# Performance work log

Measured on AMD Instinct MI355X. Metric: run time of the kernel, lower is better.

Reference implementation:

```python
import jax, jax.numpy as jnp
import numpy as np

N = 50000
E = 800000
D_IN = 128
D_H = 128
D_OUT = 128
EPS = 1e-5


def setup_inputs() -> dict:
    key = jax.random.key(0)
    ks = jax.random.split(key, 16)
    s = 1.0 / np.sqrt(D_IN)
    inp = {
        "x": jax.random.normal(ks[0], (N, D_IN), dtype=jnp.float32),
        "src": jax.random.randint(ks[1], (E,), 0, N, dtype=jnp.int32),
        "dst": jax.random.randint(ks[2], (E,), 0, N, dtype=jnp.int32),
        # SAGEConv layer 1 (in->hidden): fc_self, fc_neigh, bias
        "Ws1": jax.random.uniform(ks[3], (D_IN, D_H), jnp.float32, -s, s),
        "Wn1": jax.random.uniform(ks[4], (D_IN, D_H), jnp.float32, -s, s),
        "b1": jnp.zeros((D_H,), jnp.float32),
        # BN1
        "gamma1": jnp.ones((D_H,), jnp.float32),
        "beta1": jnp.zeros((D_H,), jnp.float32),
        # SAGEConv layer 2 (hidden->hidden)
        "Ws2": jax.random.uniform(ks[5], (D_H, D_H), jnp.float32, -s, s),
        "Wn2": jax.random.uniform(ks[6], (D_H, D_H), jnp.float32, -s, s),
        "b2": jnp.zeros((D_H,), jnp.float32),
        # BN2
        "gamma2": jnp.ones((D_H,), jnp.float32),
        "beta2": jnp.zeros((D_H,), jnp.float32),
        # SAGEConv layer 3 (hidden->out)
        "Ws3": jax.random.uniform(ks[7], (D_H, D_OUT), jnp.float32, -s, s),
        "Wn3": jax.random.uniform(ks[8], (D_H, D_OUT), jnp.float32, -s, s),
        "b3": jnp.zeros((D_OUT,), jnp.float32),
    }
    return inp


def _sage_conv(x, src, dst, Ws, Wn, b):
    # mean aggregation of neighbor (src) features onto dst nodes
    agg = jax.ops.segment_sum(x[src], dst, num_segments=N)  # [N, d]
    deg = jax.ops.segment_sum(jnp.ones((E,), x.dtype), dst, num_segments=N)
    h_neigh = agg / jnp.maximum(deg, 1.0)[:, None]  # isolated nodes -> 0
    return x @ Ws + h_neigh @ Wn + b


def _batch_norm(h, gamma, beta):
    mu = jnp.mean(h, axis=0)
    var = jnp.mean(jnp.square(h - mu), axis=0)  # biased var (torch BN)
    return (h - mu) * jax.lax.rsqrt(var + EPS) * gamma + beta


def reference(x, src, dst, Ws1, Wn1, b1, gamma1, beta1,
              Ws2, Wn2, b2, gamma2, beta2, Ws3, Wn3, b3):
    h = jax.nn.relu(_batch_norm(_sage_conv(x, src, dst, Ws1, Wn1, b1), gamma1, beta1))
    # dropout is identity at inference
    h = jax.nn.relu(_batch_norm(_sage_conv(h, src, dst, Ws2, Wn2, b2), gamma2, beta2))
    return _sage_conv(h, src, dst, Ws3, Wn3, b3)
```

## Files before the change

### kernel.cpp

```cpp
#include <hip/hip_runtime.h>

#define N_NODES 50000
#define NEDGE   800000
#define D       128
#define EPS     1e-5f
#define NT      3125
#define NUNITS  800000
#define NHALF   ((size_t)N_NODES * 64)

typedef __attribute__((ext_vector_type(8))) short bf16x8;
typedef __attribute__((ext_vector_type(4))) float f32x4;
typedef __attribute__((ext_vector_type(8))) unsigned short u16x8;

__device__ inline uint32_t bfhi(float f) {
    uint32_t u = __float_as_uint(f);
    u += 0x7fffu + ((u >> 16) & 1u);
    return u >> 16;
}
__device__ inline float bff(uint32_t h) { return __uint_as_float(h << 16); }

__global__ __launch_bounds__(256) void k_deg(const int* __restrict__ dst,
                                             int* __restrict__ degi) {
    int e = blockIdx.x * 256 + threadIdx.x;
    if (e < NEDGE) atomicAdd(&degi[dst[e]], 1);
}

__global__ __launch_bounds__(256) void k_scan1(const int* __restrict__ degi,
                                               int* __restrict__ offs,
                                               int* __restrict__ bsum) {
    __shared__ int s[256];
    int tid = threadIdx.x;
    int i = blockIdx.x * 256 + tid;
    int v = (i < N_NODES) ? degi[i] : 0;
    s[tid] = v;
    __syncthreads();
    for (int d = 1; d < 256; d <<= 1) {
        int t = (tid >= d) ? s[tid - d] : 0;
        __syncthreads();
        s[tid] += t;
        __syncthreads();
    }
    if (i < N_NODES) offs[i] = s[tid] - v;
    if (tid == 255) bsum[blockIdx.x] = s[255];
}

__global__ __launch_bounds__(256) void k_scan2(int* __restrict__ bsum, int nb) {
    __shared__ int s[256];
    int tid = threadIdx.x;
    int v = (tid < nb) ? bsum[tid] : 0;
    s[tid] = v;
    __syncthreads();
    for (int d = 1; d < 256; d <<= 1) {
        int t = (tid >= d) ? s[tid - d] : 0;
        __syncthreads();
        s[tid] += t;
        __syncthreads();
    }
    if (tid < nb) bsum[tid] = s[tid] - v;
}

__global__ __launch_bounds__(256) void k_scan3(const int* __restrict__ degi,
                                               const int* __restrict__ bsum,
                                               int* __restrict__ offs,
                                               int* __restrict__ cursor,
                                               float* __restrict__ invdeg) {
    int i = blockIdx.x * 256 + threadIdx.x;
    if (i < N_NODES) {
        int o = offs[i] + bsum[blockIdx.x];
        offs[i] = o;
        cursor[i] = o;
        int dg = degi[i];
        invdeg[i] = 1.0f / (float)(dg > 0 ? dg : 1);
    }
    if (i == 0 && blockIdx.x == 0) offs[N_NODES] = NEDGE;
}

__global__ __launch_bounds__(256) void k_fill(const int* __restrict__ src,
                                              const int* __restrict__ dst,
                                              int* __restrict__ cursor,
                                              int* __restrict__ csr) {
    int e = blockIdx.x * 256 + threadIdx.x;
    if (e < NEDGE) {
        int p = atomicAdd(&cursor[dst[e]], 1);
        csr[p] = src[e];
    }
}

__global__ __launch_bounds__(256) void k_tobf16(const float* __restrict__ X,
                                                unsigned short* __restrict__ PH,
                                                unsigned short* __restrict__ PL,
                                                unsigned short* __restrict__ XG) {
    int flat = blockIdx.x * 256 + threadIdx.x;
    if (flat >= NUNITS) return;
    int tb = flat >> 8;
    int kc = (flat >> 6) & 3;
    int l = flat & 63;
    int row = tb * 16 + (l & 15);
    int col = kc * 32 + (l >> 4) * 8;
    const float* p = X + (size_t)row * D + col;
    float4 a = *reinterpret_cast<const float4*>(p);
    float4 b = *reinterpret_cast<const float4*>(p + 4);
    float f[8] = {a.x, a.y, a.z, a.w, b.x, b.y, b.z, b.w};
    u16x8 oh, ol;
#pragma unroll
    for (int i = 0; i < 8; ++i) {
        uint32_t h = bfhi(f[i]);
        oh[i] = (unsigned short)h;
        ol[i] = (unsigned short)bfhi(f[i] - bff(h));
    }
    *reinterpret_cast<u16x8*>(PH + (size_t)flat * 8) = oh;
    *reinterpret_cast<u16x8*>(PL + (size_t)flat * 8) = ol;
    *reinterpret_cast<u16x8*>(XG + (size_t)(col >> 6) * NHALF + (size_t)row * 64 + (col & 63)) = oh;
}

__global__ __launch_bounds__(256) void k_act(const float* __restrict__ H,
                                             const float* __restrict__ scale,
                                             const float* __restrict__ shift,
                                             unsigned short* __restrict__ PH,
                                             unsigned short* __restrict__ PL,
                                             unsigned short* __restrict__ XG) {
    int flat = blockIdx.x * 256 + threadIdx.x;
    if (flat >= NUNITS) return;
    int tb = flat >> 8;
    int kc = (flat >> 6) & 3;
    int l = flat & 63;
    int row = tb * 16 + (l & 15);
    int col = kc * 32 + (l >> 4) * 8;
    const float* p = H + (size_t)row * D + col;
    float4 a = *reinterpret_cast<const float4*>(p);
    float4 b = *reinterpret_cast<const float4*>(p + 4);
    float4 s0 = *reinterpret_cast<const float4*>(scale + col);
    float4 s1 = *reinterpret_cast<const float4*>(scale + col + 4);
    float4 h0 = *reinterpret_cast<const float4*>(shift + col);
    float4 h1 = *reinterpret_cast<const float4*>(shift + col + 4);
    float f[8];
    f[0] = fmaxf(a.x * s0.x + h0.x, 0.f); f[1] = fmaxf(a.y * s0.y + h0.y, 0.f);
    f[2] = fmaxf(a.z * s0.z + h0.z, 0.f); f[3] = fmaxf(a.w * s0.w + h0.w, 0.f);
    f[4] = fmaxf(b.x * s1.x + h1.x, 0.f); f[5] = fmaxf(b.y * s1.y + h1.y, 0.f);
    f[6] = fmaxf(b.z * s1.z + h1.z, 0.f); f[7] = fmaxf(b.w * s1.w + h1.w, 0.f);
    u16x8 oh, ol;
#pragma unroll
    for (int i = 0; i < 8; ++i) {
        uint32_t h = bfhi(f[i]);
        oh[i] = (unsigned short)h;
        ol[i] = (unsigned short)bfhi(f[i] - bff(h));
    }
    *reinterpret_cast<u16x8*>(PH + (size_t)flat * 8) = oh;
    *reinterpret_cast<u16x8*>(PL + (size_t)flat * 8) = ol;
    *reinterpret_cast<u16x8*>(XG + (size_t)(col >> 6) * NHALF + (size_t)row * 64 + (col & 63)) = oh;
}

__global__ __launch_bounds__(256) void k_agg(const unsigned short* __restrict__ XG,
                                             const int* __restrict__ offs,
                                             const int* __restrict__ csr,
                                             const float* __restrict__ invdeg,
                                             unsigned short* __restrict__ HNH,
                                             unsigned short* __restrict__ HNL) {
    int bid = blockIdx.x;
    int half = (bid >> 2) & 1;
    int nb = (bid >> 3) * 4 + (bid & 3);
    if (nb >= 1563) return;
    int n = nb * 32 + (threadIdx.x >> 3);
    if (n >= N_NODES) return;
    int c = (threadIdx.x & 7) * 8;
    const unsigned short* XP = XG + (size_t)half * NHALF;

    int e0 = offs[n], e1 = offs[n + 1];
    float a0[8], a1[8];
#pragma unroll
    for (int i = 0; i < 8; ++i) { a0[i] = 0.f; a1[i] = 0.f; }

    int e = e0;
    for (; e + 2 <= e1; e += 2) {
        int s0i = csr[e], s1i = csr[e + 1];
        u16x8 v0 = *reinterpret_cast<const u16x8*>(XP + (size_t)s0i * 64 + c);
        u16x8 v1 = *reinterpret_cast<const u16x8*>(XP + (size_t)s1i * 64 + c);
#pragma unroll
        for (int i = 0; i < 8; ++i) {
            a0[i] += bff((unsigned short)v0[i]);
            a1[i] += bff((unsigned short)v1[i]);
        }
    }
    if (e < e1) {
        int s0i = csr[e];
        u16x8 v0 = *reinterpret_cast<const u16x8*>(XP + (size_t)s0i * 64 + c);
#pragma unroll
        for (int i = 0; i < 8; ++i)
            a0[i] += bff((unsigned short)v0[i]);
    }
    float id = invdeg[n];
    u16x8 oh, ol;
#pragma unroll
    for (int i = 0; i < 8; ++i) {
        float m = (a0[i] + a1[i]) * id;
        uint32_t h = bfhi(m);
        oh[i] = (unsigned short)h;
        ol[i] = (unsigned short)bfhi(m - bff(h));
    }
    int gc = half * 64 + c;
    int kc = gc >> 5;
    int l = (n & 15) + ((gc >> 3) & 3) * 16;
    size_t unit = ((size_t)(n >> 4) * 4 + kc) * 64 + l;
    *reinterpret_cast<u16x8*>(HNH + unit * 8) = oh;
    *reinterpret_cast<u16x8*>(HNL + unit * 8) = ol;
}

__global__ __launch_bounds__(256) void k_wprep(const float* __restrict__ W0,
                                               const float* __restrict__ W1,
                                               const float* __restrict__ W2,
                                               const float* __restrict__ W3,
                                               const float* __restrict__ W4,
                                               const float* __restrict__ W5,
                                               unsigned short* __restrict__ wt) {
    int mat = blockIdx.x >> 6;
    const float* srcs[6] = {W0, W1, W2, W3, W4, W5};
    const float* W = srcs[mat];
    int t = (blockIdx.x & 63) * 256 + threadIdx.x;
    int k = t >> 7;
    int n = t & 127;
    float w = W[k * 128 + n];
    uint32_t h = bfhi(w);
    uint32_t l = bfhi(w - bff(h));
    unsigned short* base = wt + (size_t)mat * 32768;
    base[n * 128 + k] = (unsigned short)h;
    base[16384 + n * 128 + k] = (unsigned short)l;
}

__global__ __launch_bounds__(256, 4) void k_mm(const unsigned short* __restrict__ PH,
                                               const unsigned short* __restrict__ PL,
                                               const unsigned short* __restrict__ HNH,
                                               const unsigned short* __restrict__ HNL,
                                               const unsigned short* __restrict__ WsT,
                                               const unsigned short* __restrict__ WnT,
                                               const float* __restrict__ bias,
                                               float* __restrict__ OUT,
                                               int doStats,
                                               float* __restrict__ sums) {
    const int tid = threadIdx.x;
    const int lane = tid & 63;
    const int wave = tid >> 6;
    const int mlo = lane & 15;
    const int g = lane >> 4;
    const int ch = blockIdx.x & 1;
    const int t0 = (blockIdx.x >> 1) * 4;
    const int row0 = t0 * 16;
    const int col = ch * 64 + wave * 16 + mlo;
    const float bcol = bias[col];

    f32x4 acc[4];
#pragma unroll
    for (int s = 0; s < 4; ++s) acc[s] = (f32x4){0.f, 0.f, 0.f, 0.f};

#pragma unroll
    for (int kc = 0; kc < 4; ++kc) {
        int ko = kc * 32 + g * 8;
        bf16x8 wsh = *reinterpret_cast<const bf16x8*>(WsT + (size_t)col * 128 + ko);
        bf16x8 wsl = *reinterpret_cast<const bf16x8*>(WsT + 16384 + (size_t)col * 128 + ko);
        bf16x8 wnh = *reinterpret_cast<const bf16x8*>(WnT + (size_t)col * 128 + ko);
        bf16x8 wnl = *reinterpret_cast<const bf16x8*>(WnT + 16384 + (size_t)col * 128 + ko);
#pragma unroll
        for (int s = 0; s < 4; ++s) {
            int t = t0 + s;
            u16x8 xh, xl, ah, al;
            if (t < NT) {
                size_t idx = (((size_t)t * 4 + kc) * 64 + lane) * 8;
                xh = *reinterpret_cast<const u16x8*>(PH + idx);
                xl = *reinterpret_cast<const u16x8*>(PL + idx);
                ah = *reinterpret_cast<const u16x8*>(HNH + idx);
                al = *reinterpret_cast<const u16x8*>(HNL + idx);
            } else {
                u16x8 z = {0, 0, 0, 0, 0, 0, 0, 0};
                xh = z; xl = z; ah = z; al = z;
            }
            bf16x8 bxh = *(bf16x8*)&xh, bxl = *(bf16x8*)&xl;
            bf16x8 bah = *(bf16x8*)&ah, bal = *(bf16x8*)&al;
            acc[s] = __builtin_amdgcn_mfma_f32_16x16x32_bf16(bxh, wsh, acc[s], 0, 0, 0);
            acc[s] = __builtin_amdgcn_mfma_f32_16x16x32_bf16(bxh, wsl, acc[s], 0, 0, 0);
            acc[s] = __builtin_amdgcn_mfma_f32_16x16x32_bf16(bxl, wsh, acc[s], 0, 0, 0);
            acc[s] = __builtin_amdgcn_mfma_f32_16x16x32_bf16(bah, wnh, acc[s], 0, 0, 0);
            acc[s] = __builtin_amdgcn_mfma_f32_16x16x32_bf16(bah, wnl, acc[s], 0, 0, 0);
            acc[s] = __builtin_amdgcn_mfma_f32_16x16x32_bf16(bal, wnh, acc[s], 0, 0, 0);
        }
    }

    float cs = 0.f, cq = 0.f;
#pragma unroll
    for (int s = 0; s < 4; ++s) {
#pragma unroll
        for (int r = 0; r < 4; ++r) {
            int grow = row0 + s * 16 + g * 4 + r;
            if (grow < N_NODES) {
                float v = acc[s][r] + bcol;
                OUT[(size_t)grow * D + col] = v;
                cs += v; cq += v * v;
            }
        }
    }
    if (doStats) {
        cs += __shfl_xor(cs, 16); cs += __shfl_xor(cs, 32);
        cq += __shfl_xor(cq, 16); cq += __shfl_xor(cq, 32);
        if (lane < 16) {
            atomicAdd(&sums[col], cs);
            atomicAdd(&sums[128 + col], cq);
        }
    }
}

__global__ void k_bnfin(const float* __restrict__ sums,
                        const float* __restrict__ gamma,
                        const float* __restrict__ beta,
                        float* __restrict__ scale,
                        float* __restrict__ shift) {
    int c = threadIdx.x;
    const float invN = 1.0f / (float)N_NODES;
    float mu = sums[c] * invN;
    float var = sums[128 + c] * invN - mu * mu;
    float s = gamma[c] * rsqrtf(var + EPS);
    scale[c] = s;
    shift[c] = beta[c] - mu * s;
}

extern "C" void kernel_launch(void* const* d_in, const int* in_sizes, int n_in,
                              void* d_out, int out_size, void* d_ws, size_t ws_size,
                              hipStream_t stream) {
    const float* x   = (const float*)d_in[0];
    const int*   src = (const int*)d_in[1];
    const int*   dst = (const int*)d_in[2];
    const float* Ws1 = (const float*)d_in[3];
    const float* Wn1 = (const float*)d_in[4];
    const float* b1  = (const float*)d_in[5];
    const float* g1  = (const float*)d_in[6];
    const float* be1 = (const float*)d_in[7];
    const float* Ws2 = (const float*)d_in[8];
    const float* Wn2 = (const float*)d_in[9];
    const float* b2  = (const float*)d_in[10];
    const float* g2  = (const float*)d_in[11];
    const float* be2 = (const float*)d_in[12];
    const float* Ws3 = (const float*)d_in[13];
    const float* Wn3 = (const float*)d_in[14];
    const float* b3  = (const float*)d_in[15];
    float* out = (float*)d_out;

    char* p = (char*)d_ws;
    auto alloc = [&](size_t bytes) -> char* {
        char* r = p;
        p += (bytes + 255) & ~(size_t)255;
        return r;
    };
    unsigned short* pfh = (unsigned short*)alloc((size_t)NUNITS * 16);
    unsigned short* pfl = (unsigned short*)alloc((size_t)NUNITS * 16);
    unsigned short* xg  = (unsigned short*)alloc((size_t)N_NODES * D * 2);
    unsigned short* hnh = (unsigned short*)alloc((size_t)NUNITS * 16);
    unsigned short* hnl = (unsigned short*)alloc((size_t)NUNITS * 16);
    float* hbuf   = (float*)alloc((size_t)N_NODES * D * 4);
    int*   csr    = (int*)alloc((size_t)NEDGE * 4);
    int*   offs   = (int*)alloc((size_t)(N_NODES + 1) * 4);
    int*   cursor = (int*)alloc((size_t)N_NODES * 4);
    int*   degi   = (int*)alloc((size_t)N_NODES * 4);
    float* invdeg = (float*)alloc((size_t)N_NODES * 4);
    int*   bsum   = (int*)alloc(1024);
    float* sums   = (float*)alloc(256 * 4);
    float* scale  = (float*)alloc(128 * 4);
    float* shift  = (float*)alloc(128 * 4);
    unsigned short* wt = (unsigned short*)alloc((size_t)6 * 32768 * 2);

    const int NB_E = (NEDGE + 255) / 256;
    const int NB_N = (N_NODES + 255) / 256;
    const int NB_A = 3128;
    const int NB_M = 2 * ((N_NODES + 63) / 64);
    const int NB_T = (NUNITS + 255) / 256;

    const unsigned short* WsT1 = wt + 0 * 32768;
    const unsigned short* WnT1 = wt + 1 * 32768;
    const unsigned short* WsT2 = wt + 2 * 32768;
    const unsigned short* WnT2 = wt + 3 * 32768;
    const unsigned short* WsT3 = wt + 4 * 32768;
    const unsigned short* WnT3 = wt + 5 * 32768;

    k_wprep<<<384, 256, 0, stream>>>(Ws1, Wn1, Ws2, Wn2, Ws3, Wn3, wt);
    hipMemsetAsync(degi, 0, (size_t)N_NODES * 4, stream);
    k_deg<<<NB_E, 256, 0, stream>>>(dst, degi);
    k_scan1<<<NB_N, 256, 0, stream>>>(degi, offs, bsum);
    k_scan2<<<1, 256, 0, stream>>>(bsum, NB_N);
    k_scan3<<<NB_N, 256, 0, stream>>>(degi, bsum, offs, cursor, invdeg);
    k_fill<<<NB_E, 256, 0, stream>>>(src, dst, cursor, csr);
    k_tobf16<<<NB_T, 256, 0, stream>>>(x, pfh, pfl, xg);

    k_agg<<<NB_A, 256, 0, stream>>>(xg, offs, csr, invdeg, hnh, hnl);
    hipMemsetAsync(sums, 0, 256 * 4, stream);
    k_mm<<<NB_M, 256, 0, stream>>>(pfh, pfl, hnh, hnl, WsT1, WnT1, b1, hbuf, 1, sums);
    k_bnfin<<<1, 128, 0, stream>>>(sums, g1, be1, scale, shift);
    k_act<<<NB_T, 256, 0, stream>>>(hbuf, scale, shift, pfh, pfl, xg);

    k_agg<<<NB_A, 256, 0, stream>>>(xg, offs, csr, invdeg, hnh, hnl);
    hipMemsetAsync(sums, 0, 256 * 4, stream);
    k_mm<<<NB_M, 256, 0, stream>>>(pfh, pfl, hnh, hnl, WsT2, WnT2, b2, hbuf, 1, sums);
    k_bnfin<<<1, 128, 0, stream>>>(sums, g2, be2, scale, shift);
    k_act<<<NB_T, 256, 0, stream>>>(hbuf, scale, shift, pfh, pfl, xg);

    k_agg<<<NB_A, 256, 0, stream>>>(xg, offs, csr, invdeg, hnh, hnl);
    k_mm<<<NB_M, 256, 0, stream>>>(pfh, pfl, hnh, hnl, WsT3, WnT3, b3, out, 0, sums);
}
```

Baseline: 427.0 us.

## Fold degree count, memsets and BN finalize into neighbouring kernels to cut launches

Degree counting moves into the bf16 conversion kernel (NUNITS equals NEDGE, so one atomic per thread). Zeroing of the degree and BN-sum buffers moves into the weight-prep kernel, which removes the memsets. The BN finalize kernel is dropped, and each k_act thread now recomputes mean, variance and scale from the sums. The fill kernel handles four edges per thread with fewer blocks. Together this removes about seven launches and memsets, at the cost of redundant per-element rsqrt work and an atomic-heavy conversion kernel.

After: 433.0 us. No clear change (+1.4%).

```diff
diff --git a/kernel.cpp b/kernel.cpp
--- a/kernel.cpp
+++ b/kernel.cpp
@@ -7,6 +7,7 @@
 #define NT      3125
 #define NUNITS  800000
 #define NHALF   ((size_t)N_NODES * 64)
+#define FILL_T  200192
 
 typedef __attribute__((ext_vector_type(8))) short bf16x8;
 typedef __attribute__((ext_vector_type(4))) float f32x4;
@@ -18,12 +19,6 @@
     return u >> 16;
 }
 __device__ inline float bff(uint32_t h) { return __uint_as_float(h << 16); }
-
-__global__ __launch_bounds__(256) void k_deg(const int* __restrict__ dst,
-                                             int* __restrict__ degi) {
-    int e = blockIdx.x * 256 + threadIdx.x;
-    if (e < NEDGE) atomicAdd(&degi[dst[e]], 1);
-}
 
 __global__ __launch_bounds__(256) void k_scan1(const int* __restrict__ degi,
                                                int* __restrict__ offs,
@@ -79,19 +74,26 @@
                                               const int* __restrict__ dst,
                                               int* __restrict__ cursor,
                                               int* __restrict__ csr) {
-    int e = blockIdx.x * 256 + threadIdx.x;
-    if (e < NEDGE) {
-        int p = atomicAdd(&cursor[dst[e]], 1);
-        csr[p] = src[e];
+    int gid = blockIdx.x * 256 + threadIdx.x;
+#pragma unroll
+    for (int it = 0; it < 4; ++it) {
+        int e = gid + it * FILL_T;
+        if (e < NEDGE) {
+            int p = atomicAdd(&cursor[dst[e]], 1);
+            csr[p] = src[e];
+        }
     }
 }
 
 __global__ __launch_bounds__(256) void k_tobf16(const float* __restrict__ X,
                                                 unsigned short* __restrict__ PH,
                                                 unsigned short* __restrict__ PL,
-                                                unsigned short* __restrict__ XG) {
+                                                unsigned short* __restrict__ XG,
+                                                const int* __restrict__ dst,
+                                                int* __restrict__ degi) {
     int flat = blockIdx.x * 256 + threadIdx.x;
     if (flat >= NUNITS) return;
+    atomicAdd(&degi[dst[flat]], 1);
     int tb = flat >> 8;
     int kc = (flat >> 6) & 3;
     int l = flat & 63;
@@ -114,8 +116,9 @@
 }
 
 __global__ __launch_bounds__(256) void k_act(const float* __restrict__ H,
-                                             const float* __restrict__ scale,
-                                             const float* __restrict__ shift,
+                                             const float* __restrict__ sums,
+                                             const float* __restrict__ gamma,
+                                             const float* __restrict__ beta,
                                              unsigned short* __restrict__ PH,
                                              unsigned short* __restrict__ PL,
                                              unsigned short* __restrict__ XG) {
@@ -126,24 +129,34 @@
     int l = flat & 63;
     int row = tb * 16 + (l & 15);
     int col = kc * 32 + (l >> 4) * 8;
+    const float invN = 1.0f / (float)N_NODES;
     const float* p = H + (size_t)row * D + col;
     float4 a = *reinterpret_cast<const float4*>(p);
     float4 b = *reinterpret_cast<const float4*>(p + 4);
-    float4 s0 = *reinterpret_cast<const float4*>(scale + col);
-    float4 s1 = *reinterpret_cast<const float4*>(scale + col + 4);
-    float4 h0 = *reinterpret_cast<const float4*>(shift + col);
-    float4 h1 = *reinterpret_cast<const float4*>(shift + col + 4);
-    float f[8];
-    f[0] = fmaxf(a.x * s0.x + h0.x, 0.f); f[1] = fmaxf(a.y * s0.y + h0.y, 0.f);
-    f[2] = fmaxf(a.z * s0.z + h0.z, 0.f); f[3] = fmaxf(a.w * s0.w + h0.w, 0.f);
-    f[4] = fmaxf(b.x * s1.x + h1.x, 0.f); f[5] = fmaxf(b.y * s1.y + h1.y, 0.f);
-    f[6] = fmaxf(b.z * s1.z + h1.z, 0.f); f[7] = fmaxf(b.w * s1.w + h1.w, 0.f);
+    float hv[8] = {a.x, a.y, a.z, a.w, b.x, b.y, b.z, b.w};
+    float4 s0 = *reinterpret_cast<const float4*>(sums + col);
+    float4 s1 = *reinterpret_cast<const float4*>(sums + col + 4);
+    float4 q0 = *reinterpret_cast<const float4*>(sums + 128 + col);
+    float4 q1 = *reinterpret_cast<const float4*>(sums + 128 + col + 4);
+    float4 g0 = *reinterpret_cast<const float4*>(gamma + col);
+    float4 g1 = *reinterpret_cast<const float4*>(gamma + col + 4);
+    float4 e0 = *reinterpret_cast<const float4*>(beta + col);
+    float4 e1 = *reinterpret_cast<const float4*>(beta + col + 4);
+    float sm[8] = {s0.x, s0.y, s0.z, s0.w, s1.x, s1.y, s1.z, s1.w};
+    float sq[8] = {q0.x, q0.y, q0.z, q0.w, q1.x, q1.y, q1.z, q1.w};
+    float gm[8] = {g0.x, g0.y, g0.z, g0.w, g1.x, g1.y, g1.z, g1.w};
+    float bt[8] = {e0.x, e0.y, e0.z, e0.w, e1.x, e1.y, e1.z, e1.w};
     u16x8 oh, ol;
 #pragma unroll
     for (int i = 0; i < 8; ++i) {
-        uint32_t h = bfhi(f[i]);
+        float mu = sm[i] * invN;
+        float var = sq[i] * invN - mu * mu;
+        float sc = gm[i] * rsqrtf(var + EPS);
+        float sh = bt[i] - mu * sc;
+        float f = fmaxf(hv[i] * sc + sh, 0.f);
+        uint32_t h = bfhi(f);
         oh[i] = (unsigned short)h;
-        ol[i] = (unsigned short)bfhi(f[i] - bff(h));
+        ol[i] = (unsigned short)bfhi(f - bff(h));
     }
     *reinterpret_cast<u16x8*>(PH + (size_t)flat * 8) = oh;
     *reinterpret_cast<u16x8*>(PL + (size_t)flat * 8) = ol;
@@ -211,7 +224,13 @@
                                                const float* __restrict__ W3,
                                                const float* __restrict__ W4,
                                                const float* __restrict__ W5,
-                                               unsigned short* __restrict__ wt) {
+                                               unsigned short* __restrict__ wt,
+                                               int* __restrict__ degi,
+                                               float* __restrict__ sums1,
+                                               float* __restrict__ sums2) {
+    int gid = blockIdx.x * 256 + threadIdx.x;
+    if (gid < N_NODES) degi[gid] = 0;
+    if (gid < 256) { sums1[gid] = 0.f; sums2[gid] = 0.f; }
     int mat = blockIdx.x >> 6;
     const float* srcs[6] = {W0, W1, W2, W3, W4, W5};
     const float* W = srcs[mat];
@@ -306,20 +325,6 @@
     }
 }
 
-__global__ void k_bnfin(const float* __restrict__ sums,
-                        const float* __restrict__ gamma,
-                        const float* __restrict__ beta,
-                        float* __restrict__ scale,
-                        float* __restrict__ shift) {
-    int c = threadIdx.x;
-    const float invN = 1.0f / (float)N_NODES;
-    float mu = sums[c] * invN;
-    float var = sums[128 + c] * invN - mu * mu;
-    float s = gamma[c] * rsqrtf(var + EPS);
-    scale[c] = s;
-    shift[c] = beta[c] - mu * s;
-}
-
 extern "C" void kernel_launch(void* const* d_in, const int* in_sizes, int n_in,
                               void* d_out, int out_size, void* d_ws, size_t ws_size,
                               hipStream_t stream) {
@@ -359,16 +364,15 @@
     int*   degi   = (int*)alloc((size_t)N_NODES * 4);
     float* invdeg = (float*)alloc((size_t)N_NODES * 4);
     int*   bsum   = (int*)alloc(1024);
-    float* sums   = (float*)alloc(256 * 4);
-    float* scale  = (float*)alloc(128 * 4);
-    float* shift  = (float*)alloc(128 * 4);
+    float* sums1  = (float*)alloc(256 * 4);
+    float* sums2  = (float*)alloc(256 * 4);
     unsigned short* wt = (unsigned short*)alloc((size_t)6 * 32768 * 2);
 
-    const int NB_E = (NEDGE + 255) / 256;
     const int NB_N = (N_NODES + 255) / 256;
     const int NB_A = 3128;
     const int NB_M = 2 * ((N_NODES + 63) / 64);
     const int NB_T = (NUNITS + 255) / 256;
+    const int NB_F = 782;
 
     const unsigned short* WsT1 = wt + 0 * 32768;
     const unsigned short* WnT1 = wt + 1 * 32768;
@@ -377,27 +381,21 @@
     const unsigned short* WsT3 = wt + 4 * 32768;
     const unsigned short* WnT3 = wt + 5 * 32768;
 
-    k_wprep<<<384, 256, 0, stream>>>(Ws1, Wn1, Ws2, Wn2, Ws3, Wn3, wt);
-    hipMemsetAsync(degi, 0, (size_t)N_NODES * 4, stream);
-    k_deg<<<NB_E, 256, 0, stream>>>(dst, degi);
+    k_wprep<<<384, 256, 0, stream>>>(Ws1, Wn1, Ws2, Wn2, Ws3, Wn3, wt, degi, sums1, sums2);
+    k_tobf16<<<NB_T, 256, 0, stream>>>(x, pfh, pfl, xg, dst, degi);
     k_scan1<<<NB_N, 256, 0, stream>>>(degi, offs, bsum);
     k_scan2<<<1, 256, 0, stream>>>(bsum, NB_N);
     k_scan3<<<NB_N, 256, 0, stream>>>(degi, bsum, offs, cursor, invdeg);
-    k_fill<<<NB_E, 256, 0, stream>>>(src, dst, cursor, csr);
-    k_tobf16<<<NB_T, 256, 0, stream>>>(x, pfh, pfl, xg);
+    k_fill<<<NB_F, 256, 0, stream>>>(src, dst, cursor, csr);
 
     k_agg<<<NB_A, 256, 0, stream>>>(xg, offs, csr, invdeg, hnh, hnl);
-    hipMemsetAsync(sums, 0, 256 * 4, stream);
-    k_mm<<<NB_M, 256, 0, stream>>>(pfh, pfl, hnh, hnl, WsT1, WnT1, b1, hbuf, 1, sums);
-    k_bnfin<<<1, 128, 0, stream>>>(sums, g1, be1, scale, shift);
-    k_act<<<NB_T, 256, 0, stream>>>(hbuf, scale, shift, pfh, pfl, xg);
+    k_mm<<<NB_M, 256, 0, stream>>>(pfh, pfl, hnh, hnl, WsT1, WnT1, b1, hbuf, 1, sums1);
+    k_act<<<NB_T, 256, 0, stream>>>(hbuf, sums1, g1, be1, pfh, pfl, xg);
 
     k_agg<<<NB_A, 256, 0, stream>>>(xg, offs, csr, invdeg, hnh, hnl);
-    hipMemsetAsync(sums, 0, 256 * 4, stream);
-    k_mm<<<NB_M, 256, 0, stream>>>(pfh, pfl, hnh, hnl, WsT2, WnT2, b2, hbuf, 1, sums);
-    k_bnfin<<<1, 128, 0, stream>>>(sums, g2, be2, scale, shift);
-    k_act<<<NB_T, 256, 0, stream>>>(hbuf, scale, shift, pfh, pfl, xg);
+    k_mm<<<NB_M, 256, 0, stream>>>(pfh, pfl, hnh, hnl, WsT2, WnT2, b2, hbuf, 1, sums2);
+    k_act<<<NB_T, 256, 0, stream>>>(hbuf, sums2, g2, be2, pfh, pfl, xg);
 
     k_agg<<<NB_A, 256, 0, stream>>>(xg, offs, csr, invdeg, hnh, hnl);
-    k_mm<<<NB_M, 256, 0, stream>>>(pfh, pfl, hnh, hnl, WsT3, WnT3, b3, out, 0, sums);
-}
+    k_mm<<<NB_M, 256, 0, stream>>>(pfh, pfl, hnh, hnl, WsT3, WnT3, b3, out, 0, sums1);
+}
```
